# Performance work log

Hardware: AMD Instinct MI355X
Metric: run time of the kernel (lower is better)

Reference implementation:

```python
import jax, jax.numpy as jnp
import numpy as np

ALPHA = 0.3
N_NODES = 100000
N_EDGES = 640000
D = 128


def setup_inputs() -> dict:
    key = jax.random.key(0)
    k1, k2, k3, k4, k5 = jax.random.split(key, 5)
    return {
        "src_embedding": jax.random.normal(k1, (N_NODES, D), dtype=jnp.float32),
        "dst_embedding": jax.random.normal(k2, (N_NODES, D), dtype=jnp.float32),
        "edge_embedding": jax.random.normal(k3, (N_EDGES, D), dtype=jnp.float32),
        "src_idx": jax.random.randint(k4, (N_EDGES,), 0, N_NODES, dtype=jnp.int64) if jax.config.jax_enable_x64 else jax.random.randint(k4, (N_EDGES,), 0, N_NODES).astype(jnp.int32),
        "dst_idx": jax.random.randint(k5, (N_EDGES,), 0, N_NODES).astype(jnp.int32),
    }


def reference(src_embedding, dst_embedding, edge_embedding, src_idx, dst_idx):
    # msg[e] = src_embedding[src_idx[e]] + edge_embedding[e]   (gather + add)
    msg = src_embedding[src_idx] + edge_embedding              # [E, D]
    # segment mean over destination nodes (DGL mailbox mean reduce)
    agg_sum = jax.ops.segment_sum(msg, dst_idx, num_segments=N_NODES)   # [N, D]
    deg = jax.ops.segment_sum(jnp.ones((msg.shape[0],), msg.dtype), dst_idx,
                              num_segments=N_NODES)            # [N]
    mean = agg_sum / jnp.maximum(deg, 1.0)[:, None]
    out = ALPHA * dst_embedding + (1.0 - ALPHA) * mean
    # DGL: nodes with no incoming messages get zeros for 'agg'
    return jnp.where(deg[:, None] > 0, out, jnp.zeros_like(out))
```

## Files before the change

### kernel.cpp

```cpp
#include <hip/hip_runtime.h>
#include <hip/hip_bf16.h>

#define ALPHA 0.3f
#define D 128


__global__ void count_kernel(const int* __restrict__ dst_idx,
                             int* __restrict__ deg, int E) {
    int e = blockIdx.x * blockDim.x + threadIdx.x;
    if (e < E) atomicAdd(&deg[dst_idx[e]], 1);
}

__global__ void alloc_kernel(const int* __restrict__ deg,
                             int* __restrict__ start,
                             int* __restrict__ cursor,
                             int* __restrict__ counter, int N) {
    __shared__ int sdata[256];
    __shared__ int sbase;
    int t = threadIdx.x;
    int n = blockIdx.x * 256 + t;
    int val = (n < N) ? deg[n] : 0;
    sdata[t] = val;
    __syncthreads();
    for (int off = 1; off < 256; off <<= 1) {
        int x = 0;
        if (t >= off) x = sdata[t - off];
        __syncthreads();
        sdata[t] += x;
        __syncthreads();
    }
    if (t == 255) sbase = atomicAdd(counter, sdata[255]);
    __syncthreads();
    int excl = sdata[t] - val;
    if (n < N) {
        int s = sbase + excl;
        start[n]  = s;
        cursor[n] = s;
    }
}

__global__ void scatter_ids_kernel(const int* __restrict__ src_idx,
                                   const int* __restrict__ dst_idx,
                                   int* __restrict__ cursor,
                                   int* __restrict__ perm_e,
                                   int* __restrict__ perm_s, int E) {
    int e = blockIdx.x * blockDim.x + threadIdx.x;
    if (e >= E) return;
    int d = dst_idx[e];
    int pos = atomicAdd(&cursor[d], 1);
    perm_e[pos] = e;
    perm_s[pos] = src_idx[e];
}

__global__ void gather_finalize_kernel(const float* __restrict__ src_emb,
                                       const float* __restrict__ dst_emb,
                                       const float* __restrict__ edge_emb,
                                       const int* __restrict__ deg,
                                       const int* __restrict__ start,
                                       const int* __restrict__ perm_e,
                                       const int* __restrict__ perm_s,
                                       float* __restrict__ out, int N) {
    int wid = blockIdx.x * (blockDim.x >> 6) + (threadIdx.x >> 6);
    int n = __builtin_amdgcn_readfirstlane(wid);
    if (n >= N) return;
    int lane = threadIdx.x & 63;

    int d  = deg[n];
    int s0 = start[n];

    float accx = 0.f, accy = 0.f;
    for (int i = 0; i < d; ++i) {
        int eid  = perm_e[s0 + i];
        int sidx = perm_s[s0 + i];
        float2 ev = ((const float2*)(edge_emb + (size_t)eid  * D))[lane];
        float2 sv = ((const float2*)(src_emb  + (size_t)sidx * D))[lane];
        accx += ev.x + sv.x;
        accy += ev.y + sv.y;
    }

    float2 o;
    if (d > 0) {
        float2 dv = ((const float2*)(dst_emb + (size_t)n * D))[lane];
        float inv = (1.0f - ALPHA) / (float)d;
        o.x = ALPHA * dv.x + accx * inv;
        o.y = ALPHA * dv.y + accy * inv;
    } else {
        o.x = 0.f; o.y = 0.f;
    }
    ((float2*)(out + (size_t)n * D))[lane] = o;
}

extern "C" void kernel_launch(void* const* d_in, const int* in_sizes, int n_in,
                              void* d_out, int out_size, void* d_ws, size_t ws_size,
                              hipStream_t stream) {
    const float* src_emb  = (const float*)d_in[0];
    const float* dst_emb  = (const float*)d_in[1];
    const float* edge_emb = (const float*)d_in[2];
    const int*   src_idx  = (const int*)d_in[3];
    const int*   dst_idx  = (const int*)d_in[4];
    float*       out      = (float*)d_out;

    const int N = in_sizes[0] / D;
    const int E = in_sizes[3];

    int* deg     = (int*)d_ws;
    int* counter = deg + N;
    int* start   = counter + 1;
    int* cursor  = start + N;
    int* perm_e  = cursor + N;
    int* perm_s  = perm_e + E;

    hipMemsetAsync(d_ws, 0, (size_t)(N + 1) * sizeof(int), stream);

    int blkE = (E + 255) / 256;
    int blkN = (N + 255) / 256;

    count_kernel<<<blkE, 256, 0, stream>>>(dst_idx, deg, E);
    alloc_kernel<<<blkN, 256, 0, stream>>>(deg, start, cursor, counter, N);
    scatter_ids_kernel<<<blkE, 256, 0, stream>>>(src_idx, dst_idx, cursor,
                                                 perm_e, perm_s, E);

    int grid = (N + 3) / 4;
    gather_finalize_kernel<<<grid, 256, 0, stream>>>(
        src_emb, dst_emb, edge_emb, deg, start, perm_e, perm_s, out, N);
}
```

Measured before the change: 604.8 us.

## Process two nodes per wavefront with 128-bit loads, unrolled gather, packed index pairs

The gather kernel now assigns each half-wavefront to one node, so a wave handles two destination nodes. Each lane loads 16-byte vectors, and the edge loop is unrolled by four with masked, clamped indices so that more loads are in flight at once. Edge IDs and source IDs are packed into one int2 array, and start/degree into another, which halves the index loads. Edge embeddings are read and outputs written with nontemporal hints. The cost is wasted masked work when the two nodes in a wave have different degrees, and the workspace layout changes.

```diff
diff --git a/kernel.cpp b/kernel.cpp
--- a/kernel.cpp
+++ b/kernel.cpp
@@ -3,6 +3,15 @@
 
 #define ALPHA 0.3f
 #define D 128
+
+typedef float v4f __attribute__((ext_vector_type(4)));
+
+__device__ __forceinline__ v4f ldnt4(const float* p) {
+    return __builtin_nontemporal_load((const v4f*)p);
+}
+__device__ __forceinline__ v4f ld4(const float* p) {
+    return *(const v4f*)p;
+}
 
 
 __global__ void count_kernel(const int* __restrict__ dst_idx,
@@ -12,7 +21,7 @@
 }
 
 __global__ void alloc_kernel(const int* __restrict__ deg,
-                             int* __restrict__ start,
+                             int2* __restrict__ range,
                              int* __restrict__ cursor,
                              int* __restrict__ counter, int N) {
     __shared__ int sdata[256];
@@ -34,7 +43,7 @@
     int excl = sdata[t] - val;
     if (n < N) {
         int s = sbase + excl;
-        start[n]  = s;
+        range[n]  = make_int2(s, val);
         cursor[n] = s;
     }
 }
@@ -42,52 +51,68 @@
 __global__ void scatter_ids_kernel(const int* __restrict__ src_idx,
                                    const int* __restrict__ dst_idx,
                                    int* __restrict__ cursor,
-                                   int* __restrict__ perm_e,
-                                   int* __restrict__ perm_s, int E) {
+                                   int2* __restrict__ perm, int E) {
     int e = blockIdx.x * blockDim.x + threadIdx.x;
     if (e >= E) return;
     int d = dst_idx[e];
     int pos = atomicAdd(&cursor[d], 1);
-    perm_e[pos] = e;
-    perm_s[pos] = src_idx[e];
+    perm[pos] = make_int2(e, src_idx[e]);
 }
 
 __global__ void gather_finalize_kernel(const float* __restrict__ src_emb,
                                        const float* __restrict__ dst_emb,
                                        const float* __restrict__ edge_emb,
-                                       const int* __restrict__ deg,
-                                       const int* __restrict__ start,
-                                       const int* __restrict__ perm_e,
-                                       const int* __restrict__ perm_s,
+                                       const int2* __restrict__ range,
+                                       const int2* __restrict__ perm,
                                        float* __restrict__ out, int N) {
-    int wid = blockIdx.x * (blockDim.x >> 6) + (threadIdx.x >> 6);
-    int n = __builtin_amdgcn_readfirstlane(wid);
-    if (n >= N) return;
+    int wid  = blockIdx.x * (blockDim.x >> 6) + (threadIdx.x >> 6);
     int lane = threadIdx.x & 63;
+    int half = lane >> 5;
+    int hl   = lane & 31;
+    int n    = 2 * wid + half;
+    bool valid = n < N;
+    int nc   = valid ? n : 0;
 
-    int d  = deg[n];
-    int s0 = start[n];
+    int2 rg = range[nc];
+    int s0  = rg.x;
+    int d   = valid ? rg.y : 0;
+    int fo  = 4 * hl;
 
-    float accx = 0.f, accy = 0.f;
-    for (int i = 0; i < d; ++i) {
-        int eid  = perm_e[s0 + i];
-        int sidx = perm_s[s0 + i];
-        float2 ev = ((const float2*)(edge_emb + (size_t)eid  * D))[lane];
-        float2 sv = ((const float2*)(src_emb  + (size_t)sidx * D))[lane];
-        accx += ev.x + sv.x;
-        accy += ev.y + sv.y;
+    int dA = __shfl(d, 0);
+    int dB = __shfl(d, 32);
+    int dmax = max(dA, dB);
+
+    v4f acc = {0.f, 0.f, 0.f, 0.f};
+
+    for (int i = 0; i < dmax; i += 4) {
+#pragma unroll
+        for (int j = 0; j < 4; ++j) {
+            int ij  = i + j;
+            int idx = (ij < d) ? ij : (d - 1);
+            float m = (ij < d) ? 1.f : 0.f;
+            int pos = (d > 0) ? (s0 + idx) : 0;
+            int2 p  = perm[pos];
+            v4f ev = ldnt4(edge_emb + (size_t)p.x * D + fo);
+            v4f sv = ld4  (src_emb  + (size_t)p.y * D + fo);
+            acc.x = fmaf(m, ev.x + sv.x, acc.x);
+            acc.y = fmaf(m, ev.y + sv.y, acc.y);
+            acc.z = fmaf(m, ev.z + sv.z, acc.z);
+            acc.w = fmaf(m, ev.w + sv.w, acc.w);
+        }
     }
 
-    float2 o;
+    v4f o = {0.f, 0.f, 0.f, 0.f};
     if (d > 0) {
-        float2 dv = ((const float2*)(dst_emb + (size_t)n * D))[lane];
+        v4f dv = ld4(dst_emb + (size_t)nc * D + fo);
         float inv = (1.0f - ALPHA) / (float)d;
-        o.x = ALPHA * dv.x + accx * inv;
-        o.y = ALPHA * dv.y + accy * inv;
-    } else {
-        o.x = 0.f; o.y = 0.f;
+        o.x = ALPHA * dv.x + acc.x * inv;
+        o.y = ALPHA * dv.y + acc.y * inv;
+        o.z = ALPHA * dv.z + acc.z * inv;
+        o.w = ALPHA * dv.w + acc.w * inv;
     }
-    ((float2*)(out + (size_t)n * D))[lane] = o;
+    if (valid) {
+        __builtin_nontemporal_store(o, (v4f*)(out + (size_t)n * D + fo));
+    }
 }
 
 extern "C" void kernel_launch(void* const* d_in, const int* in_sizes, int n_in,
@@ -103,24 +128,23 @@
     const int N = in_sizes[0] / D;
     const int E = in_sizes[3];
 
-    int* deg     = (int*)d_ws;
-    int* counter = deg + N;
-    int* start   = counter + 1;
-    int* cursor  = start + N;
-    int* perm_e  = cursor + N;
-    int* perm_s  = perm_e + E;
+    int2* perm    = (int2*)d_ws;
+    int2* range   = perm + E;
+    int*  deg     = (int*)(range + N);
+    int*  counter = deg + N;
+    int*  cursor  = counter + 1;
 
-    hipMemsetAsync(d_ws, 0, (size_t)(N + 1) * sizeof(int), stream);
+    hipMemsetAsync(deg, 0, (size_t)(N + 1) * sizeof(int), stream);
 
     int blkE = (E + 255) / 256;
     int blkN = (N + 255) / 256;
 
     count_kernel<<<blkE, 256, 0, stream>>>(dst_idx, deg, E);
-    alloc_kernel<<<blkN, 256, 0, stream>>>(deg, start, cursor, counter, N);
+    alloc_kernel<<<blkN, 256, 0, stream>>>(deg, range, cursor, counter, N);
     scatter_ids_kernel<<<blkE, 256, 0, stream>>>(src_idx, dst_idx, cursor,
-                                                 perm_e, perm_s, E);
+                                                 perm, E);
 
-    int grid = (N + 3) / 4;
+    int grid = (N + 7) / 8;
     gather_finalize_kernel<<<grid, 256, 0, stream>>>(
-        src_emb, dst_emb, edge_emb, deg, start, perm_e, perm_s, out, N);
+        src_emb, dst_emb, edge_emb, range, perm, out, N);
 }
```

Result: faster. 582.0 us (-3.8%).
